# Kernel optimization log

Measured on AMD Instinct MI355X. Metric: run time of the kernel, lower is better.

The kernel has to match this reference:

```python
import jax, jax.numpy as jnp
import numpy as np

B, T, C = 2, 2048, 768
N_HEADS = 12
D_K = C // N_HEADS  # 64


def setup_inputs() -> dict:
    key = jax.random.key(0)
    k1, k2, k3, k4, k5 = jax.random.split(key, 5)
    x = jax.random.normal(k1, (B, T, C), dtype=jnp.float32)
    # glorot-normal-ish scaled params
    query_mat = jax.random.normal(k2, (C, N_HEADS, D_K), dtype=jnp.float32) * (2.0 / (C + D_K)) ** 0.5
    key_mat = jax.random.normal(k3, (C, N_HEADS, D_K), dtype=jnp.float32) * (2.0 / (C + D_K)) ** 0.5
    value_mat = jax.random.normal(k4, (C, N_HEADS, D_K), dtype=jnp.float32) * (2.0 / (C + D_K)) ** 0.5
    linear_m1 = jax.random.normal(k5, (C, C), dtype=jnp.float32) * (2.0 / (C + C)) ** 0.5
    return {"x": x, "query_mat": query_mat, "key_mat": key_mat,
            "value_mat": value_mat, "linear_m1": linear_m1}


def reference(x, query_mat, key_mat, value_mat, linear_m1):
    b, t, c = x.shape
    h, d_k = query_mat.shape[1], query_mat.shape[2]
    q = jnp.einsum('btc,chd->bhtd', x, query_mat)
    k = jnp.einsum('btc,chd->bhtd', x, key_mat)
    v = jnp.einsum('btc,chd->bhtd', x, value_mat)
    # NOTE: original module MULTIPLIES by sqrt(d_k) (not divides) - kept faithful.
    w = jnp.einsum('bhtd,bhzd->bhtz', q, k) * (d_k ** 0.5)
    causal = jnp.tril(jnp.ones((t, t), dtype=bool))  # [T,T], True on/below diag
    w = jnp.where(causal, w, -jnp.inf)
    w = jax.nn.softmax(w, axis=-1)
    o = jnp.einsum('bhtz,bhzd->bhtd', w, v)
    o = jnp.transpose(o, (0, 2, 1, 3)).reshape(b, t, h * d_k)
    return jnp.einsum('btc,cz->btz', o, linear_m1)
```

## Files before the change

### kernel.cpp

```cpp
#include <hip/hip_runtime.h>
#include <hip/hip_bf16.h>


typedef float f32x4 __attribute__((ext_vector_type(4)));
typedef short s16x8 __attribute__((ext_vector_type(8)));

#define MFMA(a, b, c) __builtin_amdgcn_mfma_f32_16x16x32_bf16((a), (b), (c), 0, 0, 0)

constexpr int Bb = 2, Tt = 2048, Cc = 768, Hh = 12, Dd = 64;
constexpr int Mm = Bb * Tt;
constexpr int BH = Bb * Hh;

__device__ __forceinline__ void gload16(const void* g, void* l) {
  __builtin_amdgcn_global_load_lds((const __attribute__((address_space(1))) void*)g,
                                   (__attribute__((address_space(3))) void*)l, 16, 0, 0);
}

__device__ __forceinline__ short f2bfbits(float f) {
  __hip_bfloat16 h = __float2bfloat16(f);
  return __builtin_bit_cast(short, h);
}
__device__ __forceinline__ float bf2f(short s) {
  __hip_bfloat16 h = __builtin_bit_cast(__hip_bfloat16, s);
  return __bfloat162float(h);
}
__device__ __forceinline__ unsigned int packbf2(float a, float b) {
  return (unsigned int)(unsigned short)f2bfbits(a) |
         ((unsigned int)(unsigned short)f2bfbits(b) << 16);
}

#if __has_builtin(__builtin_amdgcn_exp2f)
__device__ __forceinline__ float fexp2(float x) { return __builtin_amdgcn_exp2f(x); }
#else
__device__ __forceinline__ float fexp2(float x) {
  float r;
  asm("v_exp_f32 %0, %1" : "=v"(r) : "v"(x));
  return r;
}
#endif

__global__ __launch_bounds__(256) void prep_all(
    const float* __restrict__ x,
    const float* __restrict__ s0, const float* __restrict__ s1,
    const float* __restrict__ s2, const float* __restrict__ s3,
    __hip_bfloat16* __restrict__ xhi, __hip_bfloat16* __restrict__ xlo,
    __hip_bfloat16* __restrict__ h0, __hip_bfloat16* __restrict__ l0,
    __hip_bfloat16* __restrict__ h1, __hip_bfloat16* __restrict__ l1,
    __hip_bfloat16* __restrict__ h2, __hip_bfloat16* __restrict__ h3) {
  __shared__ float tile[64][65];
  const int bid = blockIdx.x;
  if (bid < 1536) {
    const size_t i = ((size_t)bid * 256 + threadIdx.x) * 8;
    float4 a = *reinterpret_cast<const float4*>(x + i);
    float4 b = *reinterpret_cast<const float4*>(x + i + 4);
    float v[8] = {a.x, a.y, a.z, a.w, b.x, b.y, b.z, b.w};
    s16x8 hi, lo;
#pragma unroll
    for (int j = 0; j < 8; ++j) {
      short h = f2bfbits(v[j]);
      hi[j] = h;
      lo[j] = f2bfbits(v[j] - bf2f(h));
    }
    *reinterpret_cast<s16x8*>((short*)xhi + i) = hi;
    *reinterpret_cast<s16x8*>((short*)xlo + i) = lo;
    return;
  }
  const int q = bid - 1536;
  const int z = q / 144, rem = q % 144;
  const int by = rem / 12, bx = rem % 12;
  const float* src;
  __hip_bfloat16 *dh, *dl = nullptr;
  switch (z) {
    case 0: src = s0; dh = h0; dl = l0; break;
    case 1: src = s1; dh = h1; dl = l1; break;
    case 2: src = s2; dh = h2; break;
    default: src = s3; dh = h3; break;
  }
  const int r0 = by * 64, c0 = bx * 64;
  const int tid = threadIdx.x;
  const int rr = tid >> 4, c4 = (tid & 15) * 4;
#pragma unroll
  for (int it = 0; it < 4; ++it) {
    float4 v = *reinterpret_cast<const float4*>(src + (size_t)(r0 + rr + it * 16) * Cc + c0 + c4);
    tile[rr + it * 16][c4 + 0] = v.x;
    tile[rr + it * 16][c4 + 1] = v.y;
    tile[rr + it * 16][c4 + 2] = v.z;
    tile[rr + it * 16][c4 + 3] = v.w;
  }
  __syncthreads();
#pragma unroll
  for (int it = 0; it < 2; ++it) {
    const int id = tid + it * 256;
    const int n = id >> 3, ch = (id & 7) * 8;
    s16x8 hi, lo;
#pragma unroll
    for (int j = 0; j < 8; ++j) {
      float v = tile[ch + j][n];
      short h = f2bfbits(v);
      hi[j] = h;
      lo[j] = f2bfbits(v - bf2f(h));
    }
    *reinterpret_cast<s16x8*>(dh + (size_t)(c0 + n) * Cc + r0 + ch) = hi;
    if (dl) *reinterpret_cast<s16x8*>(dl + (size_t)(c0 + n) * Cc + r0 + ch) = lo;
  }
}

__device__ __forceinline__ void gemm128_core(const __hip_bfloat16* __restrict__ A,
                                             const __hip_bfloat16* __restrict__ Bt,
                                             int m0, int n0,
                                             short* ldsA, short* ldsB,
                                             f32x4 acc[4][4]) {
  const int tid = threadIdx.x;
  const int w = tid >> 6, l = tid & 63;
  const int wr = w >> 1, wc = w & 1;
  const int srow = l >> 2;
  const int scol = (l & 3) << 3;

  for (int kt = 0; kt < Cc / 32; ++kt) {
    const int kk = kt << 5;
#pragma unroll
    for (int i = 0; i < 2; ++i) {
      const int r = (w << 5) + (i << 4);
      gload16(A + (size_t)(m0 + r + srow) * Cc + kk + scol, ldsA + r * 32);
      gload16(Bt + (size_t)(n0 + r + srow) * Cc + kk + scol, ldsB + r * 32);
    }
    __syncthreads();
    s16x8 af[4], bfr[4];
#pragma unroll
    for (int i = 0; i < 4; ++i) {
      af[i]  = *reinterpret_cast<const s16x8*>(ldsA + ((wr << 6) + (i << 4) + (l & 15)) * 32 + ((l >> 4) << 3));
      bfr[i] = *reinterpret_cast<const s16x8*>(ldsB + ((wc << 6) + (i << 4) + (l & 15)) * 32 + ((l >> 4) << 3));
    }
#pragma unroll
    for (int i = 0; i < 4; ++i)
#pragma unroll
      for (int j = 0; j < 4; ++j)
        acc[i][j] = MFMA(af[i], bfr[j], acc[i][j]);
    __syncthreads();
  }
}

__device__ __forceinline__ void gemm128_hilo(
    const __hip_bfloat16* __restrict__ Ahi, const __hip_bfloat16* __restrict__ Alo,
    const __hip_bfloat16* __restrict__ Bhi, const __hip_bfloat16* __restrict__ Blo,
    bool lo, int m0, int n0, short* lds, f32x4 acc[4][4]) {
  short* ldsAh = lds;
  short* ldsAl = lds + 4096;
  short* ldsBh = lds + 8192;
  short* ldsBl = lds + 12288;
  const int tid = threadIdx.x;
  const int w = tid >> 6, l = tid & 63;
  const int wr = w >> 1, wc = w & 1;
  const int srow = l >> 2;
  const int scol = (l & 3) << 3;

  for (int kt = 0; kt < Cc / 32; ++kt) {
    const int kk = kt << 5;
#pragma unroll
    for (int i = 0; i < 2; ++i) {
      const int r = (w << 5) + (i << 4);
      const size_t aoff = (size_t)(m0 + r + srow) * Cc + kk + scol;
      const size_t boff = (size_t)(n0 + r + srow) * Cc + kk + scol;
      gload16(Ahi + aoff, ldsAh + r * 32);
      gload16(Bhi + boff, ldsBh + r * 32);
      if (lo) {
        gload16(Alo + aoff, ldsAl + r * 32);
        gload16(Blo + boff, ldsBl + r * 32);
      }
    }
    __syncthreads();
    s16x8 ah[4], bh[4], al[4], bl[4];
#pragma unroll
    for (int i = 0; i < 4; ++i) {
      const int ao = ((wr << 6) + (i << 4) + (l & 15)) * 32 + ((l >> 4) << 3);
      const int bo = ((wc << 6) + (i << 4) + (l & 15)) * 32 + ((l >> 4) << 3);
      ah[i] = *reinterpret_cast<const s16x8*>(ldsAh + ao);
      bh[i] = *reinterpret_cast<const s16x8*>(ldsBh + bo);
      if (lo) {
        al[i] = *reinterpret_cast<const s16x8*>(ldsAl + ao);
        bl[i] = *reinterpret_cast<const s16x8*>(ldsBl + bo);
      }
    }
#pragma unroll
    for (int i = 0; i < 4; ++i)
#pragma unroll
      for (int j = 0; j < 4; ++j)
        acc[i][j] = MFMA(ah[i], bh[j], acc[i][j]);
    if (lo) {
#pragma unroll
      for (int i = 0; i < 4; ++i)
#pragma unroll
        for (int j = 0; j < 4; ++j) {
          acc[i][j] = MFMA(ah[i], bl[j], acc[i][j]);
          acc[i][j] = MFMA(al[i], bh[j], acc[i][j]);
        }
    }
    __syncthreads();
  }
}

__global__ __launch_bounds__(256) void qkv_gemm(
    const __hip_bfloat16* __restrict__ Xhi, const __hip_bfloat16* __restrict__ Xlo,
    const __hip_bfloat16* __restrict__ WqThi, const __hip_bfloat16* __restrict__ WqTlo,
    const __hip_bfloat16* __restrict__ WkThi, const __hip_bfloat16* __restrict__ WkTlo,
    const __hip_bfloat16* __restrict__ WvThi,
    __hip_bfloat16* __restrict__ Qhi, __hip_bfloat16* __restrict__ Qlo,
    __hip_bfloat16* __restrict__ Khi, __hip_bfloat16* __restrict__ Klo,
    __hip_bfloat16* __restrict__ VT) {
  __shared__ __align__(16) short lds[16384];
  const int z = blockIdx.z;
  const bool lo = (z < 2);
  const __hip_bfloat16* Bhi = (z == 0) ? WqThi : (z == 1) ? WkThi : WvThi;
  const __hip_bfloat16* Blo = (z == 0) ? WqTlo : WkTlo;
  const int m0 = blockIdx.x * 128, n0 = blockIdx.y * 128;

  f32x4 acc[4][4];
#pragma unroll
  for (int i = 0; i < 4; ++i)
#pragma unroll
    for (int j = 0; j < 4; ++j) acc[i][j] = f32x4{0.f, 0.f, 0.f, 0.f};

  gemm128_hilo(Xhi, Xlo, Bhi, Blo, lo, m0, n0, lds, acc);

  const int tid = threadIdx.x, w = tid >> 6, l = tid & 63;
  const int wr = w >> 1, wc = w & 1;
  if (z == 2) {
#pragma unroll
    for (int i = 0; i < 4; ++i)
#pragma unroll
      for (int j = 0; j < 4; ++j) {
        const int mb = m0 + (wr << 6) + (i << 4) + ((l >> 4) << 2);
        const int n = n0 + (wc << 6) + (j << 4) + (l & 15);
        const int b = mb >> 11, t0 = mb & 2047, h = n >> 6, d = n & 63;
        uint2 pk;
        pk.x = packbf2(acc[i][j][0], acc[i][j][1]);
        pk.y = packbf2(acc[i][j][2], acc[i][j][3]);
        *reinterpret_cast<uint2*>(
            (short*)VT + ((size_t)(b * Hh + h) * Dd + d) * Tt + t0) = pk;
      }
    return;
  }
#pragma unroll
  for (int i = 0; i < 4; ++i) {
#pragma unroll
    for (int j = 0; j < 4; ++j) {
#pragma unroll
      for (int r = 0; r < 4; ++r) {
        const int m = m0 + (wr << 6) + (i << 4) + ((l >> 4) << 2) + r;
        const int n = n0 + (wc << 6) + (j << 4) + (l & 15);
        float v = acc[i][j][r];
        const int b = m >> 11, t = m & 2047, h = n >> 6, d = n & 63;
        const size_t idx = (((size_t)(b * Hh + h)) * Tt + t) * Dd + d;
        if (z == 0) v *= 11.5415603f;
        short hbits = f2bfbits(v);
        short lbits = f2bfbits(v - bf2f(hbits));
        if (z == 0) { ((short*)Qhi)[idx] = hbits; ((short*)Qlo)[idx] = lbits; }
        else        { ((short*)Khi)[idx] = hbits; ((short*)Klo)[idx] = lbits; }
      }
    }
  }
}

__global__ __launch_bounds__(256) void proj_gemm(
    const __hip_bfloat16* __restrict__ O, const __hip_bfloat16* __restrict__ LT,
    float* __restrict__ out) {
  __shared__ __align__(16) short lds[8192];
  const int m0 = blockIdx.x * 128, n0 = blockIdx.y * 128;
  f32x4 acc[4][4];
#pragma unroll
  for (int i = 0; i < 4; ++i)
#pragma unroll
    for (int j = 0; j < 4; ++j) acc[i][j] = f32x4{0.f, 0.f, 0.f, 0.f};

  gemm128_core(O, LT, m0, n0, lds, lds + 4096, acc);

  const int tid = threadIdx.x, w = tid >> 6, l = tid & 63;
  const int wr = w >> 1, wc = w & 1;
#pragma unroll
  for (int i = 0; i < 4; ++i)
#pragma unroll
    for (int j = 0; j < 4; ++j)
#pragma unroll
      for (int r = 0; r < 4; ++r) {
        const int m = m0 + (wr << 6) + (i << 4) + ((l >> 4) << 2) + r;
        const int n = n0 + (wc << 6) + (j << 4) + (l & 15);
        out[(size_t)m * Cc + n] = acc[i][j][r];
      }
}

__global__ __launch_bounds__(256, 3) void attn_fwd(
    const __hip_bfloat16* __restrict__ Qhi, const __hip_bfloat16* __restrict__ Qlo,
    const __hip_bfloat16* __restrict__ Khi, const __hip_bfloat16* __restrict__ Klo,
    const __hip_bfloat16* __restrict__ VT, __hip_bfloat16* __restrict__ O) {
  __shared__ __align__(16) short kvk[2][2][4096];
  __shared__ __align__(16) short kvv[4096];
  __shared__ __align__(16) short pbuf[4][16 * 72];
  const int i = blockIdx.x;
  const int j = i >> 3;
  const int m3 = j >> 5;
  const int bh = (i & 7) * 3 + m3;
  const int s_ = j & 31;
  const int h1t[8] = {3, 4, 7, 5, 2, 6, 1, 0};
  const int h2t[8] = {7, 6, 1, 2, 5, 0, 3, 4};
  const int p1t[4] = {2, 3, 1, 0};
  const int p2t[4] = {3, 0, 2, 1};
  const int qblk = (m3 == 0) ? s_
                 : (m3 == 1) ? 4 * h1t[s_ >> 2] + p1t[s_ & 3]
                             : 4 * h2t[s_ >> 2] + p2t[s_ & 3];
  const int b = bh / Hh, h = bh % Hh;
  const int tid = threadIdx.x, w = tid >> 6, l = tid & 63;
  const int lr = l & 15, lg = l >> 4;
  const int q0 = qblk * 64 + w * 16;
  const size_t hqk = (size_t)bh * Tt * Dd;
  const __hip_bfloat16* qhp = Qhi + hqk;
  const __hip_bfloat16* qlp = Qlo + hqk;
  const __hip_bfloat16* khp = Khi + hqk;
  const __hip_bfloat16* klp = Klo + hqk;
  const __hip_bfloat16* vtp = VT + (size_t)bh * Dd * Tt;
  short* myP = &pbuf[w][0];
  short* obase = (short*)O + (size_t)b * Tt * Cc + h * Dd;

  const int rr = l >> 3;
  const int gg = (l & 7) ^ rr;

  auto stageK = [&](int buf, int k0) {
#pragma unroll
    for (int s6 = 0; s6 < 4; ++s6) {
      const int s = w * 4 + s6;
      const int m = s >> 3, i2 = s & 7;
      const int row = i2 * 8 + rr;
      const __hip_bfloat16* src = (m == 0)
          ? khp + (size_t)(k0 + row) * Dd + gg * 8
          : klp + (size_t)(k0 + row) * Dd + gg * 8;
      gload16(src, &kvk[buf][m][i2 * 512]);
    }
  };
  auto stageV = [&](int k0) {
#pragma unroll
    for (int s6 = 0; s6 < 2; ++s6) {
      const int i2 = w * 2 + s6;
      const int row = i2 * 8 + rr;
      gload16(vtp + (size_t)row * Tt + k0 + gg * 8, &kvv[i2 * 512]);
    }
  };

  stageK(0, 0);
  stageV(0);

  s16x8 qh[2], ql[2];
#pragma unroll
  for (int df = 0; df < 2; ++df) {
    const size_t off = (size_t)(q0 + lr) * Dd + df * 32 + lg * 8;
    qh[df] = *reinterpret_cast<const s16x8*>(qhp + off);
    ql[df] = *reinterpret_cast<const s16x8*>(qlp + off);
  }

  f32x4 oacc[4];
#pragma unroll
  for (int df = 0; df < 4; ++df) oacc[df] = f32x4{0.f, 0.f, 0.f, 0.f};
  float mrow = -__builtin_inff(), lrow = 0.f;

  __syncthreads();

  const int sw = lr & 7;
  const int nt = qblk;
  for (int kt = 0; kt <= nt; ++kt) {
    const int cur = kt & 1;
    const int k0 = kt << 6;
    if (kt > 0) stageV(k0);
    if (kt < nt) stageK(cur ^ 1, (kt + 1) << 6);

    const short* Kh = &kvk[cur][0][0];
    const short* Kl = &kvk[cur][1][0];

    f32x4 s[4];
#pragma unroll
    for (int kjf = 0; kjf < 4; ++kjf) s[kjf] = f32x4{0.f, 0.f, 0.f, 0.f};
#pragma unroll
    for (int kjf = 0; kjf < 4; ++kjf)
#pragma unroll
      for (int df = 0; df < 2; ++df) {
        const int off = (kjf * 16 + lr) * 64 + (((df * 4 + lg) ^ sw) << 3);
        const s16x8 kh = *reinterpret_cast<const s16x8*>(Kh + off);
        const s16x8 kl = *reinterpret_cast<const s16x8*>(Kl + off);
        s[kjf] = MFMA(kh, qh[df], s[kjf]);
        s[kjf] = MFMA(kl, qh[df], s[kjf]);
        s[kjf] = MFMA(kh, ql[df], s[kjf]);
      }

    const int q = q0 + lr;
    const bool dotmask = (k0 + 63) > q0;
    float mx = -__builtin_inff();
#pragma unroll
    for (int kjf = 0; kjf < 4; ++kjf)
#pragma unroll
      for (int r = 0; r < 4; ++r) {
        float v = s[kjf][r];
        if (dotmask && (k0 + kjf * 16 + lg * 4 + r) > q) v = -__builtin_inff();
        s[kjf][r] = v;
        mx = fmaxf(mx, v);
      }
    mx = fmaxf(mx, __shfl_xor(mx, 16));
    mx = fmaxf(mx, __shfl_xor(mx, 32));
    if (!__all(mx <= mrow + 8.0f)) {
      const float mnew = fmaxf(mrow, mx);
      const float sc = fexp2(mrow - mnew);
      mrow = mnew;
      lrow *= sc;
#pragma unroll
      for (int df = 0; df < 4; ++df) oacc[df] *= sc;
    }
    float ls = 0.f;
#pragma unroll
    for (int kjf = 0; kjf < 4; ++kjf)
#pragma unroll
      for (int r = 0; r < 4; ++r) {
        const float p = fexp2(s[kjf][r] - mrow);
        s[kjf][r] = p;
        ls += p;
      }
    ls += __shfl_xor(ls, 16);
    ls += __shfl_xor(ls, 32);
    lrow += ls;

#pragma unroll
    for (int kjf = 0; kjf < 4; ++kjf) {
      uint2 pk;
      pk.x = packbf2(s[kjf][0], s[kjf][1]);
      pk.y = packbf2(s[kjf][2], s[kjf][3]);
      *reinterpret_cast<uint2*>(myP + lr * 72 + kjf * 16 + lg * 4) = pk;
    }

    if (kt < nt) {
      asm volatile("s_waitcnt vmcnt(4)" ::: "memory");
    } else {
      asm volatile("s_waitcnt vmcnt(0)" ::: "memory");
    }
    __builtin_amdgcn_sched_barrier(0);

#pragma unroll
    for (int kf = 0; kf < 2; ++kf) {
      const s16x8 pa = *reinterpret_cast<const s16x8*>(myP + lr * 72 + kf * 32 + lg * 8);
#pragma unroll
      for (int df = 0; df < 4; ++df) {
        const int off = (df * 16 + lr) * 64 + (((kf * 4 + lg) ^ sw) << 3);
        const s16x8 bv = *reinterpret_cast<const s16x8*>(kvv + off);
        oacc[df] = MFMA(bv, pa, oacc[df]);
      }
    }

    __syncthreads();
  }

  const float inv = 1.0f / lrow;
  const int t = q0 + lr;
#pragma unroll
  for (int df = 0; df < 4; ++df) {
    uint2 pk;
    pk.x = packbf2(oacc[df][0] * inv, oacc[df][1] * inv);
    pk.y = packbf2(oacc[df][2] * inv, oacc[df][3] * inv);
    *reinterpret_cast<uint2*>(obase + (size_t)t * Cc + df * 16 + lg * 4) = pk;
  }
}

extern "C" void kernel_launch(void* const* d_in, const int* in_sizes, int n_in,
                              void* d_out, int out_size, void* d_ws, size_t ws_size,
                              hipStream_t stream) {
  (void)in_sizes; (void)n_in; (void)out_size; (void)ws_size;
  const float* x  = (const float*)d_in[0];
  const float* wq = (const float*)d_in[1];
  const float* wk = (const float*)d_in[2];
  const float* wv = (const float*)d_in[3];
  const float* lm = (const float*)d_in[4];
  float* out = (float*)d_out;
  __hip_bfloat16* ws = (__hip_bfloat16*)d_ws;

  const size_t WSZ = (size_t)Cc * Cc;
  const size_t TSZ = (size_t)Mm * Cc;
  __hip_bfloat16* WqThi = ws;
  __hip_bfloat16* WqTlo = WqThi + WSZ;
  __hip_bfloat16* WkThi = WqTlo + WSZ;
  __hip_bfloat16* WkTlo = WkThi + WSZ;
  __hip_bfloat16* WvThi = WkTlo + WSZ;
  __hip_bfloat16* LThi  = WvThi + WSZ;
  __hip_bfloat16* Xhi   = LThi + WSZ;
  __hip_bfloat16* Xlo   = Xhi + TSZ;
  __hip_bfloat16* Qhi   = Xlo + TSZ;
  __hip_bfloat16* Qlo   = Qhi + TSZ;
  __hip_bfloat16* Khi   = Qlo + TSZ;
  __hip_bfloat16* Klo   = Khi + TSZ;
  __hip_bfloat16* Vb    = Klo + TSZ;
  __hip_bfloat16* VT    = Vb + TSZ;
  __hip_bfloat16* Ob    = Vb;

  prep_all<<<dim3(2112), 256, 0, stream>>>(x, wq, wk, wv, lm, Xhi, Xlo,
                                           WqThi, WqTlo, WkThi, WkTlo, WvThi, LThi);
  qkv_gemm<<<dim3(32, 6, 3), 256, 0, stream>>>(Xhi, Xlo, WqThi, WqTlo, WkThi, WkTlo,
                                               WvThi, Qhi, Qlo, Khi, Klo, VT);
  attn_fwd<<<dim3(768), 256, 0, stream>>>(Qhi, Qlo, Khi, Klo, VT, Ob);
  proj_gemm<<<dim3(32, 6), 256, 0, stream>>>(Ob, LThi, out);
}
```

Measured before the change: 119.1 us.

## Fuse Q and K projections into one kernel sharing X tiles; split V GEMM

Replaces the single z-indexed QKV GEMM launch with a fused Q+K kernel that loads each X hi/lo tile once and accumulates both Q and K outputs, plus a separate V kernel using the plain bf16 GEMM core. This halves X tile loads for Q/K and removes the per-block branching on the lo path. The cost is doubled accumulator registers (two 4x4 f32x4 sets), a larger LDS footprint, a grid of only 192 blocks for the fused kernel, and one extra kernel launch.

```diff
diff --git a/kernel.cpp b/kernel.cpp
--- a/kernel.cpp
+++ b/kernel.cpp
@@ -140,20 +140,29 @@
   }
 }
 
-__device__ __forceinline__ void gemm128_hilo(
-    const __hip_bfloat16* __restrict__ Ahi, const __hip_bfloat16* __restrict__ Alo,
-    const __hip_bfloat16* __restrict__ Bhi, const __hip_bfloat16* __restrict__ Blo,
-    bool lo, int m0, int n0, short* lds, f32x4 acc[4][4]) {
-  short* ldsAh = lds;
-  short* ldsAl = lds + 4096;
-  short* ldsBh = lds + 8192;
-  short* ldsBl = lds + 12288;
+__global__ __launch_bounds__(256, 2) void qk_gemm(
+    const __hip_bfloat16* __restrict__ Xhi, const __hip_bfloat16* __restrict__ Xlo,
+    const __hip_bfloat16* __restrict__ WqThi, const __hip_bfloat16* __restrict__ WqTlo,
+    const __hip_bfloat16* __restrict__ WkThi, const __hip_bfloat16* __restrict__ WkTlo,
+    __hip_bfloat16* __restrict__ Qhi, __hip_bfloat16* __restrict__ Qlo,
+    __hip_bfloat16* __restrict__ Khi, __hip_bfloat16* __restrict__ Klo) {
+  __shared__ __align__(16) short lds[24576];
+  const int m0 = blockIdx.x * 128, n0 = blockIdx.y * 128;
   const int tid = threadIdx.x;
   const int w = tid >> 6, l = tid & 63;
   const int wr = w >> 1, wc = w & 1;
   const int srow = l >> 2;
   const int scol = (l & 3) << 3;
 
+  f32x4 aq[4][4], ak[4][4];
+#pragma unroll
+  for (int i = 0; i < 4; ++i)
+#pragma unroll
+    for (int j = 0; j < 4; ++j) {
+      aq[i][j] = f32x4{0.f, 0.f, 0.f, 0.f};
+      ak[i][j] = f32x4{0.f, 0.f, 0.f, 0.f};
+    }
+
   for (int kt = 0; kt < Cc / 32; ++kt) {
     const int kk = kt << 5;
 #pragma unroll
@@ -161,85 +170,58 @@
       const int r = (w << 5) + (i << 4);
       const size_t aoff = (size_t)(m0 + r + srow) * Cc + kk + scol;
       const size_t boff = (size_t)(n0 + r + srow) * Cc + kk + scol;
-      gload16(Ahi + aoff, ldsAh + r * 32);
-      gload16(Bhi + boff, ldsBh + r * 32);
-      if (lo) {
-        gload16(Alo + aoff, ldsAl + r * 32);
-        gload16(Blo + boff, ldsBl + r * 32);
-      }
+      gload16(Xhi   + aoff, lds +     0 + r * 32);
+      gload16(Xlo   + aoff, lds +  4096 + r * 32);
+      gload16(WqThi + boff, lds +  8192 + r * 32);
+      gload16(WqTlo + boff, lds + 12288 + r * 32);
+      gload16(WkThi + boff, lds + 16384 + r * 32);
+      gload16(WkTlo + boff, lds + 20480 + r * 32);
     }
     __syncthreads();
-    s16x8 ah[4], bh[4], al[4], bl[4];
+    s16x8 ah[4], al[4];
 #pragma unroll
     for (int i = 0; i < 4; ++i) {
       const int ao = ((wr << 6) + (i << 4) + (l & 15)) * 32 + ((l >> 4) << 3);
-      const int bo = ((wc << 6) + (i << 4) + (l & 15)) * 32 + ((l >> 4) << 3);
-      ah[i] = *reinterpret_cast<const s16x8*>(ldsAh + ao);
-      bh[i] = *reinterpret_cast<const s16x8*>(ldsBh + bo);
-      if (lo) {
-        al[i] = *reinterpret_cast<const s16x8*>(ldsAl + ao);
-        bl[i] = *reinterpret_cast<const s16x8*>(ldsBl + bo);
-      }
-    }
-#pragma unroll
-    for (int i = 0; i < 4; ++i)
-#pragma unroll
-      for (int j = 0; j < 4; ++j)
-        acc[i][j] = MFMA(ah[i], bh[j], acc[i][j]);
-    if (lo) {
+      ah[i] = *reinterpret_cast<const s16x8*>(lds +    0 + ao);
+      al[i] = *reinterpret_cast<const s16x8*>(lds + 4096 + ao);
+    }
+    {
+      s16x8 bh[4], bl[4];
+#pragma unroll
+      for (int j = 0; j < 4; ++j) {
+        const int bo = ((wc << 6) + (j << 4) + (l & 15)) * 32 + ((l >> 4) << 3);
+        bh[j] = *reinterpret_cast<const s16x8*>(lds +  8192 + bo);
+        bl[j] = *reinterpret_cast<const s16x8*>(lds + 12288 + bo);
+      }
 #pragma unroll
       for (int i = 0; i < 4; ++i)
 #pragma unroll
         for (int j = 0; j < 4; ++j) {
-          acc[i][j] = MFMA(ah[i], bl[j], acc[i][j]);
-          acc[i][j] = MFMA(al[i], bh[j], acc[i][j]);
+          aq[i][j] = MFMA(ah[i], bh[j], aq[i][j]);
+          aq[i][j] = MFMA(ah[i], bl[j], aq[i][j]);
+          aq[i][j] = MFMA(al[i], bh[j], aq[i][j]);
         }
     }
+    {
+      s16x8 bh[4], bl[4];
+#pragma unroll
+      for (int j = 0; j < 4; ++j) {
+        const int bo = ((wc << 6) + (j << 4) + (l & 15)) * 32 + ((l >> 4) << 3);
+        bh[j] = *reinterpret_cast<const s16x8*>(lds + 16384 + bo);
+        bl[j] = *reinterpret_cast<const s16x8*>(lds + 20480 + bo);
+      }
+#pragma unroll
+      for (int i = 0; i < 4; ++i)
+#pragma unroll
+        for (int j = 0; j < 4; ++j) {
+          ak[i][j] = MFMA(ah[i], bh[j], ak[i][j]);
+          ak[i][j] = MFMA(ah[i], bl[j], ak[i][j]);
+          ak[i][j] = MFMA(al[i], bh[j], ak[i][j]);
+        }
+    }
     __syncthreads();
   }
-}
-
-__global__ __launch_bounds__(256) void qkv_gemm(
-    const __hip_bfloat16* __restrict__ Xhi, const __hip_bfloat16* __restrict__ Xlo,
-    const __hip_bfloat16* __restrict__ WqThi, const __hip_bfloat16* __restrict__ WqTlo,
-    const __hip_bfloat16* __restrict__ WkThi, const __hip_bfloat16* __restrict__ WkTlo,
-    const __hip_bfloat16* __restrict__ WvThi,
-    __hip_bfloat16* __restrict__ Qhi, __hip_bfloat16* __restrict__ Qlo,
-    __hip_bfloat16* __restrict__ Khi, __hip_bfloat16* __restrict__ Klo,
-    __hip_bfloat16* __restrict__ VT) {
-  __shared__ __align__(16) short lds[16384];
-  const int z = blockIdx.z;
-  const bool lo = (z < 2);
-  const __hip_bfloat16* Bhi = (z == 0) ? WqThi : (z == 1) ? WkThi : WvThi;
-  const __hip_bfloat16* Blo = (z == 0) ? WqTlo : WkTlo;
-  const int m0 = blockIdx.x * 128, n0 = blockIdx.y * 128;
-
-  f32x4 acc[4][4];
-#pragma unroll
-  for (int i = 0; i < 4; ++i)
-#pragma unroll
-    for (int j = 0; j < 4; ++j) acc[i][j] = f32x4{0.f, 0.f, 0.f, 0.f};
-
-  gemm128_hilo(Xhi, Xlo, Bhi, Blo, lo, m0, n0, lds, acc);
-
-  const int tid = threadIdx.x, w = tid >> 6, l = tid & 63;
-  const int wr = w >> 1, wc = w & 1;
-  if (z == 2) {
-#pragma unroll
-    for (int i = 0; i < 4; ++i)
-#pragma unroll
-      for (int j = 0; j < 4; ++j) {
-        const int mb = m0 + (wr << 6) + (i << 4) + ((l >> 4) << 2);
-        const int n = n0 + (wc << 6) + (j << 4) + (l & 15);
-        const int b = mb >> 11, t0 = mb & 2047, h = n >> 6, d = n & 63;
-        uint2 pk;
-        pk.x = packbf2(acc[i][j][0], acc[i][j][1]);
-        pk.y = packbf2(acc[i][j][2], acc[i][j][3]);
-        *reinterpret_cast<uint2*>(
-            (short*)VT + ((size_t)(b * Hh + h) * Dd + d) * Tt + t0) = pk;
-      }
-    return;
-  }
+
 #pragma unroll
   for (int i = 0; i < 4; ++i) {
 #pragma unroll
@@ -248,17 +230,49 @@
       for (int r = 0; r < 4; ++r) {
         const int m = m0 + (wr << 6) + (i << 4) + ((l >> 4) << 2) + r;
         const int n = n0 + (wc << 6) + (j << 4) + (l & 15);
-        float v = acc[i][j][r];
         const int b = m >> 11, t = m & 2047, h = n >> 6, d = n & 63;
         const size_t idx = (((size_t)(b * Hh + h)) * Tt + t) * Dd + d;
-        if (z == 0) v *= 11.5415603f;
-        short hbits = f2bfbits(v);
-        short lbits = f2bfbits(v - bf2f(hbits));
-        if (z == 0) { ((short*)Qhi)[idx] = hbits; ((short*)Qlo)[idx] = lbits; }
-        else        { ((short*)Khi)[idx] = hbits; ((short*)Klo)[idx] = lbits; }
-      }
-    }
-  }
+        const float vq = aq[i][j][r] * 11.5415603f;
+        short qh = f2bfbits(vq);
+        ((short*)Qhi)[idx] = qh;
+        ((short*)Qlo)[idx] = f2bfbits(vq - bf2f(qh));
+        const float vk = ak[i][j][r];
+        short kh = f2bfbits(vk);
+        ((short*)Khi)[idx] = kh;
+        ((short*)Klo)[idx] = f2bfbits(vk - bf2f(kh));
+      }
+    }
+  }
+}
+
+__global__ __launch_bounds__(256) void v_gemm(
+    const __hip_bfloat16* __restrict__ Xhi, const __hip_bfloat16* __restrict__ WvThi,
+    __hip_bfloat16* __restrict__ VT) {
+  __shared__ __align__(16) short lds[8192];
+  const int m0 = blockIdx.x * 128, n0 = blockIdx.y * 128;
+  f32x4 acc[4][4];
+#pragma unroll
+  for (int i = 0; i < 4; ++i)
+#pragma unroll
+    for (int j = 0; j < 4; ++j) acc[i][j] = f32x4{0.f, 0.f, 0.f, 0.f};
+
+  gemm128_core(Xhi, WvThi, m0, n0, lds, lds + 4096, acc);
+
+  const int tid = threadIdx.x, w = tid >> 6, l = tid & 63;
+  const int wr = w >> 1, wc = w & 1;
+#pragma unroll
+  for (int i = 0; i < 4; ++i)
+#pragma unroll
+    for (int j = 0; j < 4; ++j) {
+      const int mb = m0 + (wr << 6) + (i << 4) + ((l >> 4) << 2);
+      const int n = n0 + (wc << 6) + (j << 4) + (l & 15);
+      const int b = mb >> 11, t0 = mb & 2047, h = n >> 6, d = n & 63;
+      uint2 pk;
+      pk.x = packbf2(acc[i][j][0], acc[i][j][1]);
+      pk.y = packbf2(acc[i][j][2], acc[i][j][3]);
+      *reinterpret_cast<uint2*>(
+          (short*)VT + ((size_t)(b * Hh + h) * Dd + d) * Tt + t0) = pk;
+    }
 }
 
 __global__ __launch_bounds__(256) void proj_gemm(
@@ -495,8 +509,9 @@
 
   prep_all<<<dim3(2112), 256, 0, stream>>>(x, wq, wk, wv, lm, Xhi, Xlo,
                                            WqThi, WqTlo, WkThi, WkTlo, WvThi, LThi);
-  qkv_gemm<<<dim3(32, 6, 3), 256, 0, stream>>>(Xhi, Xlo, WqThi, WqTlo, WkThi, WkTlo,
-                                               WvThi, Qhi, Qlo, Khi, Klo, VT);
+  qk_gemm<<<dim3(32, 6), 256, 0, stream>>>(Xhi, Xlo, WqThi, WqTlo, WkThi, WkTlo,
+                                           Qhi, Qlo, Khi, Klo);
+  v_gemm<<<dim3(32, 6), 256, 0, stream>>>(Xhi, WvThi, VT);
   attn_fwd<<<dim3(768), 256, 0, stream>>>(Qhi, Qlo, Khi, Klo, VT, Ob);
   proj_gemm<<<dim3(32, 6), 256, 0, stream>>>(Ob, LThi, out);
 }
```

Result: slower. 146.6 us (+23.1%).

## Split heavy causal attention query blocks across two workgroups and merge partials

Applied to the files above, without the earlier changes.

Query blocks in the upper half of the causal sequence, which carry the most key tiles, are now split into two halves of the key range, each handled by its own workgroup. Those workgroups write unnormalized fp32 accumulators plus row max and sum to workspace buffers, and a new merge kernel combines them with a log-sum-exp rescale. Light blocks still run to completion in one workgroup. This aims to balance load and shorten the tail of the attention grid, at the cost of an extra kernel launch, fp32 partial traffic, and workspace aliasing onto buffers that are no longer needed at that point.

```diff
diff --git a/kernel.cpp b/kernel.cpp
--- a/kernel.cpp
+++ b/kernel.cpp
@@ -291,22 +291,26 @@
 __global__ __launch_bounds__(256, 3) void attn_fwd(
     const __hip_bfloat16* __restrict__ Qhi, const __hip_bfloat16* __restrict__ Qlo,
     const __hip_bfloat16* __restrict__ Khi, const __hip_bfloat16* __restrict__ Klo,
-    const __hip_bfloat16* __restrict__ VT, __hip_bfloat16* __restrict__ O) {
+    const __hip_bfloat16* __restrict__ VT, __hip_bfloat16* __restrict__ O,
+    float* __restrict__ PA, float* __restrict__ PM, float* __restrict__ PL) {
   __shared__ __align__(16) short kvk[2][2][4096];
   __shared__ __align__(16) short kvv[4096];
   __shared__ __align__(16) short pbuf[4][16 * 72];
   const int i = blockIdx.x;
-  const int j = i >> 3;
-  const int m3 = j >> 5;
-  const int bh = (i & 7) * 3 + m3;
-  const int s_ = j & 31;
-  const int h1t[8] = {3, 4, 7, 5, 2, 6, 1, 0};
-  const int h2t[8] = {7, 6, 1, 2, 5, 0, 3, 4};
-  const int p1t[4] = {2, 3, 1, 0};
-  const int p2t[4] = {3, 0, 2, 1};
-  const int qblk = (m3 == 0) ? s_
-                 : (m3 == 1) ? 4 * h1t[s_ >> 2] + p1t[s_ & 3]
-                             : 4 * h2t[s_ >> 2] + p2t[s_ & 3];
+  const int u = i >> 3;
+  const int bh = (i & 7) * 3 + u / 48;
+  const int t48 = u % 48;
+  const int k = t48 / 3, r3 = t48 % 3;
+  int qblk, kt0, kt1, split;
+  if (r3 == 2) {
+    qblk = 15 - k; kt0 = 0; kt1 = qblk + 1; split = -1;
+  } else {
+    qblk = 31 - k;
+    const int hmid = (qblk + 1) >> 1;
+    split = r3;
+    kt0 = r3 ? hmid : 0;
+    kt1 = r3 ? (qblk + 1) : hmid;
+  }
   const int b = bh / Hh, h = bh % Hh;
   const int tid = threadIdx.x, w = tid >> 6, l = tid & 63;
   const int lr = l & 15, lg = l >> 4;
@@ -344,8 +348,8 @@
     }
   };
 
-  stageK(0, 0);
-  stageV(0);
+  stageK(0, kt0 << 6);
+  stageV(kt0 << 6);
 
   s16x8 qh[2], ql[2];
 #pragma unroll
@@ -363,12 +367,11 @@
   __syncthreads();
 
   const int sw = lr & 7;
-  const int nt = qblk;
-  for (int kt = 0; kt <= nt; ++kt) {
-    const int cur = kt & 1;
+  for (int kt = kt0; kt < kt1; ++kt) {
+    const int cur = (kt - kt0) & 1;
     const int k0 = kt << 6;
-    if (kt > 0) stageV(k0);
-    if (kt < nt) stageK(cur ^ 1, (kt + 1) << 6);
+    if (kt > kt0) stageV(k0);
+    if (kt + 1 < kt1) stageK(cur ^ 1, (kt + 1) << 6);
 
     const short* Kh = &kvk[cur][0][0];
     const short* Kl = &kvk[cur][1][0];
@@ -431,7 +434,7 @@
       *reinterpret_cast<uint2*>(myP + lr * 72 + kjf * 16 + lg * 4) = pk;
     }
 
-    if (kt < nt) {
+    if (kt + 1 < kt1) {
       asm volatile("s_waitcnt vmcnt(4)" ::: "memory");
     } else {
       asm volatile("s_waitcnt vmcnt(0)" ::: "memory");
@@ -452,14 +455,60 @@
     __syncthreads();
   }
 
-  const float inv = 1.0f / lrow;
-  const int t = q0 + lr;
-#pragma unroll
-  for (int df = 0; df < 4; ++df) {
+  if (split < 0) {
+    const float inv = 1.0f / lrow;
+    const int t = q0 + lr;
+#pragma unroll
+    for (int df = 0; df < 4; ++df) {
+      uint2 pk;
+      pk.x = packbf2(oacc[df][0] * inv, oacc[df][1] * inv);
+      pk.y = packbf2(oacc[df][2] * inv, oacc[df][3] * inv);
+      *reinterpret_cast<uint2*>(obase + (size_t)t * Cc + df * 16 + lg * 4) = pk;
+    }
+  } else {
+    const int pidx = ((bh * 16 + (qblk - 16)) << 1) | split;
+    const int row = w * 16 + lr;
+    float* pa = PA + (size_t)pidx * 4096 + row * 64;
+#pragma unroll
+    for (int df = 0; df < 4; ++df)
+      *reinterpret_cast<f32x4*>(pa + df * 16 + lg * 4) = oacc[df];
+    if (lg == 0) {
+      PM[pidx * 64 + row] = mrow;
+      PL[pidx * 64 + row] = lrow;
+    }
+  }
+}
+
+__global__ __launch_bounds__(256) void merge_heavy(
+    const float* __restrict__ PA, const float* __restrict__ PM,
+    const float* __restrict__ PL, __hip_bfloat16* __restrict__ O) {
+  const int bid = blockIdx.x;
+  const int bh = bid >> 4, hq = bid & 15;
+  const int qblk = 16 + hq;
+  const int b = bh / Hh, h = bh % Hh;
+  const int p0 = (bh * 16 + hq) << 1;
+  const int tid = threadIdx.x;
+  const int ro = tid >> 2;
+  const int cg = (tid & 3) << 4;
+  const float m0 = PM[p0 * 64 + ro], m1 = PM[(p0 + 1) * 64 + ro];
+  const float l0 = PL[p0 * 64 + ro], l1 = PL[(p0 + 1) * 64 + ro];
+  const float m = fmaxf(m0, m1);
+  const float w0 = fexp2(m0 - m), w1 = fexp2(m1 - m);
+  const float inv = 1.0f / (w0 * l0 + w1 * l1);
+  const float* a0 = PA + (size_t)p0 * 4096 + ro * 64 + cg;
+  const float* a1 = a0 + 4096;
+  const int t = qblk * 64 + ro;
+  short* dst = (short*)O + ((size_t)b * Tt + t) * Cc + h * Dd + cg;
+#pragma unroll
+  for (int g = 0; g < 4; ++g) {
+    float v0 = (w0 * a0[g * 4 + 0] + w1 * a1[g * 4 + 0]) * inv;
+    float v1 = (w0 * a0[g * 4 + 1] + w1 * a1[g * 4 + 1]) * inv;
+    float v2 = (w0 * a0[g * 4 + 2] + w1 * a1[g * 4 + 2]) * inv;
+    float v3 = (w0 * a0[g * 4 + 3] + w1 * a1[g * 4 + 3]) * inv;
     uint2 pk;
-    pk.x = packbf2(oacc[df][0] * inv, oacc[df][1] * inv);
-    pk.y = packbf2(oacc[df][2] * inv, oacc[df][3] * inv);
-    *reinterpret_cast<uint2*>(obase + (size_t)t * Cc + df * 16 + lg * 4) = pk;
+    pk.x = packbf2(v0, v1);
+    pk.y = packbf2(v2, v3);
+    *reinterpret_cast<uint2*>(dst + g * 4) = pk;
   }
 }
 
@@ -493,10 +542,15 @@
   __hip_bfloat16* VT    = Vb + TSZ;
   __hip_bfloat16* Ob    = Vb;
 
+  float* PA = (float*)Xhi;
+  float* PM = (float*)WqThi;
+  float* PL = (float*)WkThi;
+
   prep_all<<<dim3(2112), 256, 0, stream>>>(x, wq, wk, wv, lm, Xhi, Xlo,
                                            WqThi, WqTlo, WkThi, WkTlo, WvThi, LThi);
   qkv_gemm<<<dim3(32, 6, 3), 256, 0, stream>>>(Xhi, Xlo, WqThi, WqTlo, WkThi, WkTlo,
                                                WvThi, Qhi, Qlo, Khi, Klo, VT);
-  attn_fwd<<<dim3(768), 256, 0, stream>>>(Qhi, Qlo, Khi, Klo, VT, Ob);
+  attn_fwd<<<dim3(1152), 256, 0, stream>>>(Qhi, Qlo, Khi, Klo, VT, Ob, PA, PM, PL);
+  merge_heavy<<<dim3(384), 256, 0, stream>>>(PA, PM, PL, Ob);
   proj_gemm<<<dim3(32, 6), 256, 0, stream>>>(Ob, LThi, out);
 }
```

Result: no change. 120.4 us (+1.1%).
